# Kernel optimization log

Measured on AMD Instinct MI355X. Metric: run time of the kernel, lower is better.

Reference implementation:

```python
import jax, jax.numpy as jnp
import numpy as np

B, N, DIM, H, DH = 8, 1024, 1024, 16, 64
INNER = H * DH
GRID = 32  # 32x32 patch grid -> N=1024
EPS_LN = 1e-5
EPS_NORM = 1e-12


def _rotate_half(x):
    x1, x2 = jnp.split(x, 2, axis=-1)
    return jnp.concatenate([-x2, x1], axis=-1)


def _rope_sincos(idx, dim_quarter):
    # idx: [B, N] float -> sin/cos [B, 1, N, dim_half]
    inv_freq = 1.0 / (10000.0 ** (jnp.arange(dim_quarter, dtype=jnp.float32) / dim_quarter))
    theta = idx[..., None] * inv_freq  # [B, N, dq]
    sin = jnp.concatenate([jnp.sin(theta), jnp.sin(theta)], axis=-1)[:, None]
    cos = jnp.concatenate([jnp.cos(theta), jnp.cos(theta)], axis=-1)[:, None]
    return sin, cos


def _apply_2d_rope(q, k, h_idx, w_idx):
    D = q.shape[-1]
    dh, dq = D // 2, D // 4
    sin_h, cos_h = _rope_sincos(h_idx, dq)
    sin_w, cos_w = _rope_sincos(w_idx, dq)
    rope = lambda x, s, c: x * c + _rotate_half(x) * s
    q = jnp.concatenate([rope(q[..., :dh], sin_h, cos_h), rope(q[..., dh:], sin_w, cos_w)], axis=-1)
    k = jnp.concatenate([rope(k[..., :dh], sin_h, cos_h), rope(k[..., dh:], sin_w, cos_w)], axis=-1)
    return q, k


def setup_inputs() -> dict:
    key = jax.random.key(0)
    ks = jax.random.split(key, 8)
    x = jax.random.normal(ks[0], (B, N, DIM), dtype=jnp.float32)
    mask = jnp.ones((B, N), dtype=bool)
    ii = jnp.arange(N, dtype=jnp.float32)
    h_idx = jnp.broadcast_to(jnp.floor(ii / GRID), (B, N))
    w_idx = jnp.broadcast_to(jnp.mod(ii, GRID), (B, N))
    s = 1.0 / np.sqrt(DIM)
    return {
        "x": x,
        "mask": mask,
        "h_idx": h_idx,
        "w_idx": w_idx,
        "gamma_ln": jnp.ones((DIM,), jnp.float32),
        "beta_ln": jnp.zeros((DIM,), jnp.float32),
        "q_gamma": jnp.ones((H, 1, DH), jnp.float32),
        "k_gamma": jnp.ones((H, 1, DH), jnp.float32),
        "Wq": jax.random.normal(ks[1], (DIM, INNER), jnp.float32) * s,
        "Wkv": jax.random.normal(ks[2], (DIM, 2 * INNER), jnp.float32) * s,
        "Wo": jax.random.normal(ks[3], (INNER, DIM), jnp.float32) * s,
    }


def reference(x, mask, h_idx, w_idx, gamma_ln, beta_ln, q_gamma, k_gamma, Wq, Wkv, Wo):
    # LayerNorm (eps=1e-5, torch default)
    mu = jnp.mean(x, axis=-1, keepdims=True)
    var = jnp.var(x, axis=-1, keepdims=True)
    xn = (x - mu) * jax.lax.rsqrt(var + EPS_LN) * gamma_ln + beta_ln

    q = xn @ Wq                          # [B, N, inner]
    kv = xn @ Wkv
    k, v = jnp.split(kv, 2, axis=-1)
    split_heads = lambda t: t.reshape(B, N, H, DH).transpose(0, 2, 1, 3)  # [B,H,N,D]
    q, k, v = split_heads(q), split_heads(k), split_heads(v)

    # QK RMSNorm: F.normalize(x, dim=-1) * sqrt(D) * gamma
    scale = jnp.sqrt(jnp.float32(DH))
    l2 = lambda t: t / jnp.maximum(jnp.linalg.norm(t, axis=-1, keepdims=True), EPS_NORM)
    q = l2(q) * scale * q_gamma
    k = l2(k) * scale * k_gamma

    q, k = _apply_2d_rope(q, k, h_idx, w_idx)

    dots = jnp.einsum("bhnd,bhmd->bhnm", q, k)  # note: no 1/sqrt(d) scaling, as in source
    neg = -jnp.finfo(dots.dtype).max
    dots = jnp.where(mask[:, None, None, :], dots, neg)
    attn = jax.nn.softmax(dots, axis=-1)
    out = jnp.einsum("bhnm,bhmd->bhnd", attn, v)
    out = out.transpose(0, 2, 1, 3).reshape(B, N, INNER)
    return out @ Wo
```

## Files before the change

### kernel.cpp

```cpp
#include <hip/hip_runtime.h>
#include <math.h>


typedef float f32x4 __attribute__((ext_vector_type(4)));
typedef _Float16 f16x8 __attribute__((ext_vector_type(8)));
typedef _Float16 f16x4 __attribute__((ext_vector_type(4)));

#define MFMA16(a, b, c) __builtin_amdgcn_mfma_f32_16x16x32_f16(a, b, c, 0, 0, 0)

__device__ __forceinline__ void gl_lds16(const void* g, void* l) {
  __builtin_amdgcn_global_load_lds(
      (const __attribute__((address_space(1))) unsigned int*)g,
      (__attribute__((address_space(3))) unsigned int*)l, 16, 0, 0);
}

__global__ __launch_bounds__(256) void ln_kernel(
    const float* __restrict__ x, const float* __restrict__ gamma,
    const float* __restrict__ beta, _Float16* __restrict__ xn) {
  int row = blockIdx.x;
  const float* xr = x + (size_t)row * 1024;
  int t = threadIdx.x;
  f32x4 v = *(const f32x4*)(xr + t * 4);
  float s = v.x + v.y + v.z + v.w;
  float s2 = v.x * v.x + v.y * v.y + v.z * v.z + v.w * v.w;
#pragma unroll
  for (int off = 1; off < 64; off <<= 1) {
    s += __shfl_xor(s, off);
    s2 += __shfl_xor(s2, off);
  }
  __shared__ float red[8];
  int w = t >> 6;
  if ((t & 63) == 0) { red[w] = s; red[4 + w] = s2; }
  __syncthreads();
  s = red[0] + red[1] + red[2] + red[3];
  s2 = red[4] + red[5] + red[6] + red[7];
  float mu = s * (1.0f / 1024.0f);
  float var = s2 * (1.0f / 1024.0f) - mu * mu;
  float rs = rsqrtf(var + 1e-5f);
  f32x4 g = *(const f32x4*)(gamma + t * 4);
  f32x4 bt = *(const f32x4*)(beta + t * 4);
  f16x4 o;
  o[0] = (_Float16)((v.x - mu) * rs * g.x + bt.x);
  o[1] = (_Float16)((v.y - mu) * rs * g.y + bt.y);
  o[2] = (_Float16)((v.z - mu) * rs * g.z + bt.z);
  o[3] = (_Float16)((v.w - mu) * rs * g.w + bt.w);
  *(f16x4*)(xn + (size_t)row * 1024 + t * 4) = o;
}

__global__ __launch_bounds__(256) void transpose_f16(
    const float* __restrict__ W, _Float16* __restrict__ BT, int K, int N) {
  __shared__ _Float16 t[64][65];
  int n0 = blockIdx.x * 64, k0 = blockIdx.y * 64;
  for (int i = threadIdx.x; i < 4096; i += 256) {
    int r = i >> 6, c = i & 63;
    t[c][r] = (_Float16)W[(size_t)(k0 + r) * N + n0 + c];
  }
  __syncthreads();
  for (int i = threadIdx.x; i < 4096; i += 256) {
    int r = i >> 6, c = i & 63;
    BT[(size_t)(n0 + r) * K + k0 + c] = t[r][c];
  }
}

template <int MODE>
__global__ __launch_bounds__(256, 4) void gemm128(
    const _Float16* __restrict__ A, const _Float16* __restrict__ BT,
    float* __restrict__ Cout,
    const float* __restrict__ q_gamma, const float* __restrict__ k_gamma,
    const float* __restrict__ h_idx, const float* __restrict__ w_idx,
    _Float16* __restrict__ Qh, _Float16* __restrict__ Kh,
    _Float16* __restrict__ VT) {
  __shared__ char smem[32768];
  int tid = threadIdx.x;
  int w = tid >> 6, l = tid & 63, hi = l >> 4, lo = l & 15;
  int wm = w >> 1, wn = w & 1;
  int bcol = blockIdx.x * 128, brow = blockIdx.y * 128;
  const char* Ab = (const char*)A + (size_t)brow * 2048;
  const char* Bb = (const char*)BT + (size_t)bcol * 2048;

  auto STAGE = [&](int buf, int kt) {
    char* Ad = smem + buf * 8192;
    char* Bd = smem + 16384 + buf * 8192;
#pragma unroll
    for (int i = 0; i < 2; ++i) {
      int o = i * 4096 + w * 1024 + l * 16;
      int r = o >> 6, cb = o & 63;
      int cs = cb ^ (((r >> 1) & 3) << 4);
      gl_lds16(Ab + (size_t)r * 2048 + kt * 64 + cs, Ad + i * 4096 + w * 1024);
      gl_lds16(Bb + (size_t)r * 2048 + kt * 64 + cs, Bd + i * 4096 + w * 1024);
    }
  };

  f32x4 acc[4][4] = {};
  STAGE(0, 0);
  __syncthreads();
  for (int t = 0; t < 32; ++t) {
    int buf = t & 1;
    if (t < 31) STAGE(buf ^ 1, t + 1);
    const char* Ac = smem + buf * 8192;
    const char* Bc = smem + 16384 + buf * 8192;
    f16x8 af[4], bf[4];
#pragma unroll
    for (int m = 0; m < 4; ++m) {
      int ro = wm * 64 + m * 16 + lo;
      af[m] = *(const f16x8*)(Ac + ro * 64 + ((hi ^ ((ro >> 1) & 3)) << 4));
    }
#pragma unroll
    for (int n = 0; n < 4; ++n) {
      int ro = wn * 64 + n * 16 + lo;
      bf[n] = *(const f16x8*)(Bc + ro * 64 + ((hi ^ ((ro >> 1) & 3)) << 4));
    }
    __builtin_amdgcn_s_setprio(1);
#pragma unroll
    for (int m = 0; m < 4; ++m)
#pragma unroll
      for (int n = 0; n < 4; ++n)
        acc[m][n] = MFMA16(af[m], bf[n], acc[m][n]);
    __builtin_amdgcn_s_setprio(0);
    __syncthreads();
  }

  if constexpr (MODE == 0) {
#pragma unroll
    for (int m = 0; m < 4; ++m) {
      int r0 = brow + wm * 64 + m * 16 + hi * 4;
#pragma unroll
      for (int n = 0; n < 4; ++n) {
        int cc = bcol + wn * 64 + n * 16 + lo;
#pragma unroll
        for (int r = 0; r < 4; ++r)
          Cout[(size_t)(r0 + r) * 1024 + cc] = acc[m][n][r];
      }
    }
  } else {
    int gcol0 = bcol + wn * 64;
    if (gcol0 < 2048) {
      int head = (gcol0 & 1023) >> 6;
      const float* gm = (gcol0 < 1024 ? q_gamma : k_gamma) + head * 64;
      _Float16* dst = (gcol0 < 1024) ? Qh : Kh;
      float g0 = gm[lo], g1 = gm[16 + lo], g2 = gm[32 + lo], g3 = gm[48 + lo];
      float invf = exp2f(-13.2877123795f * (float)lo * (1.0f / 16.0f));
#pragma unroll
      for (int mf = 0; mf < 4; ++mf) {
#pragma unroll
        for (int r = 0; r < 4; ++r) {
          float v0 = acc[mf][0][r], v1 = acc[mf][1][r];
          float v2 = acc[mf][2][r], v3 = acc[mf][3][r];
          float ss = v0 * v0 + v1 * v1 + v2 * v2 + v3 * v3;
          ss += __shfl_xor(ss, 1);
          ss += __shfl_xor(ss, 2);
          ss += __shfl_xor(ss, 4);
          ss += __shfl_xor(ss, 8);
          float sc = 8.0f / fmaxf(sqrtf(ss), 1e-12f);
          float y0 = v0 * sc * g0, y1 = v1 * sc * g1;
          float y2 = v2 * sc * g2, y3 = v3 * sc * g3;
          int rr = brow + wm * 64 + mf * 16 + hi * 4 + r;
          int b = rr >> 10, tok = rr & 1023;
          float hv = h_idx[(b << 10) + tok], wv = w_idx[(b << 10) + tok];
          float sh, ch, sw2, cw;
          __sincosf(hv * invf, &sh, &ch);
          __sincosf(wv * invf, &sw2, &cw);
          _Float16* outp = dst + ((size_t)((b * 16 + head) * 1024 + tok)) * 64;
          outp[lo]      = (_Float16)(y0 * ch - y1 * sh);
          outp[16 + lo] = (_Float16)(y1 * ch + y0 * sh);
          outp[32 + lo] = (_Float16)(y2 * cw - y3 * sw2);
          outp[48 + lo] = (_Float16)(y3 * cw + y2 * sw2);
        }
      }
    } else {
      int head = (gcol0 - 2048) >> 6;
#pragma unroll
      for (int mf = 0; mf < 4; ++mf) {
        int rr0 = brow + wm * 64 + mf * 16 + hi * 4;
        int b = rr0 >> 10, tok0 = rr0 & 1023;
#pragma unroll
        for (int nf = 0; nf < 4; ++nf) {
          int d = nf * 16 + lo;
          f16x4 pk;
          pk[0] = (_Float16)acc[mf][nf][0];
          pk[1] = (_Float16)acc[mf][nf][1];
          pk[2] = (_Float16)acc[mf][nf][2];
          pk[3] = (_Float16)acc[mf][nf][3];
          *(f16x4*)(VT + ((size_t)((b * 16 + head) * 64 + d)) * 1024 + tok0) = pk;
        }
      }
    }
  }
}

__global__ __launch_bounds__(256) void flash_kernel(
    const _Float16* __restrict__ Q, const _Float16* __restrict__ Kb,
    const _Float16* __restrict__ VT, _Float16* __restrict__ AO) {
  __shared__ _Float16 Ks[2][64 * 64];
  __shared__ _Float16 Vs[2][64 * 64];
  __shared__ _Float16 Ps[4][16 * 64];
  int tid = threadIdx.x, w = tid >> 6, l = tid & 63, hi = l >> 4, lo = l & 15;
  int qt = blockIdx.x, h = blockIdx.y, b = blockIdx.z;
  int bh = (b << 4) + h;
  const _Float16* Qb = Q + (size_t)bh * 65536;
  const char* Kg = (const char*)(Kb + (size_t)bh * 65536);
  const char* Vg = (const char*)(VT + (size_t)bh * 65536);
  int qrow = qt * 64 + w * 16 + lo;
  f16x8 qf[2];
  qf[0] = *(const f16x8*)(Qb + (size_t)qrow * 64 + hi * 8);
  qf[1] = *(const f16x8*)(Qb + (size_t)qrow * 64 + 32 + hi * 8);

  int o0 = w * 1024 + l * 16;
  auto STAGE = [&](int buf, int kt) {
#pragma unroll
    for (int c = 0; c < 2; ++c) {
      int o = o0 + c * 4096;
      int row = o >> 7, col = o & 127;
      int sw = (row & 7) << 4;
      gl_lds16(Kg + (size_t)(kt * 64 + row) * 128 + (col ^ sw),
               (char*)Ks[buf] + o);
      gl_lds16(Vg + (size_t)kt * 128 + (size_t)row * 2048 + (col ^ sw),
               (char*)Vs[buf] + o);
    }
  };

  f32x4 oacc[4] = {};
  float mrun = -1e30f, lrun = 0.f;
  char* myP = (char*)Ps[w];
  int psw = (lo & 7) << 4;

  STAGE(0, 0);
  __syncthreads();
  for (int kt = 0; kt < 16; ++kt) {
    int buf = kt & 1;
    if (kt < 15) STAGE(buf ^ 1, kt + 1);
    f32x4 sacc[4] = {};
    __builtin_amdgcn_s_setprio(1);
#pragma unroll
    for (int ks = 0; ks < 2; ++ks) {
#pragma unroll
      for (int n = 0; n < 4; ++n) {
        int row = n * 16 + lo;
        f16x8 kf = *(const f16x8*)((const char*)Ks[buf] + row * 128 +
                                   ((ks * 64 + hi * 16) ^ ((row & 7) << 4)));
        sacc[n] = MFMA16(kf, qf[ks], sacc[n]);
      }
    }
    __builtin_amdgcn_s_setprio(0);
    float pmax = sacc[0][0];
#pragma unroll
    for (int n = 0; n < 4; ++n)
#pragma unroll
      for (int r = 0; r < 4; ++r) pmax = fmaxf(pmax, sacc[n][r]);
    pmax = fmaxf(pmax, __shfl_xor(pmax, 16));
    pmax = fmaxf(pmax, __shfl_xor(pmax, 32));
    float al = 1.0f;
    if (!__all(pmax <= mrun + 8.0f)) {
      float mnew = fmaxf(mrun, pmax);
      al = __expf(mrun - mnew);
      mrun = mnew;
#pragma unroll
      for (int n = 0; n < 4; ++n)
#pragma unroll
        for (int r = 0; r < 4; ++r) oacc[n][r] *= al;
    }
    float psum = 0.f;
    float p[4][4];
#pragma unroll
    for (int n = 0; n < 4; ++n)
#pragma unroll
      for (int r = 0; r < 4; ++r) {
        p[n][r] = __expf(sacc[n][r] - mrun);
        psum += p[n][r];
      }
    psum += __shfl_xor(psum, 16);
    psum += __shfl_xor(psum, 32);
    lrun = lrun * al + psum;
#pragma unroll
    for (int n = 0; n < 4; ++n) {
      f16x4 pk;
      pk[0] = (_Float16)p[n][0];
      pk[1] = (_Float16)p[n][1];
      pk[2] = (_Float16)p[n][2];
      pk[3] = (_Float16)p[n][3];
      *(f16x4*)(myP + lo * 128 + ((n * 32 + hi * 8) ^ psw)) = pk;
    }
    __builtin_amdgcn_s_setprio(1);
#pragma unroll
    for (int m = 0; m < 2; ++m) {
      f16x8 pb = *(const f16x8*)(myP + lo * 128 + ((m * 64 + hi * 16) ^ psw));
#pragma unroll
      for (int n = 0; n < 4; ++n) {
        int row = n * 16 + lo;
        f16x8 vf = *(const f16x8*)((const char*)Vs[buf] + row * 128 +
                                   ((m * 64 + hi * 16) ^ ((row & 7) << 4)));
        oacc[n] = MFMA16(vf, pb, oacc[n]);
      }
    }
    __builtin_amdgcn_s_setprio(0);
    __syncthreads();
  }
  float inv = 1.0f / lrun;
  int tok = qt * 64 + w * 16 + lo;
#pragma unroll
  for (int n = 0; n < 4; ++n) {
    f16x4 o4;
    o4[0] = (_Float16)(oacc[n][0] * inv);
    o4[1] = (_Float16)(oacc[n][1] * inv);
    o4[2] = (_Float16)(oacc[n][2] * inv);
    o4[3] = (_Float16)(oacc[n][3] * inv);
    *(f16x4*)(AO + ((size_t)(b * 1024) + tok) * 1024 + h * 64 + n * 16 + hi * 4) = o4;
  }
}

extern "C" void kernel_launch(void* const* d_in, const int* in_sizes, int n_in,
                              void* d_out, int out_size, void* d_ws, size_t ws_size,
                              hipStream_t stream) {
  const float* x        = (const float*)d_in[0];
  const float* h_idx    = (const float*)d_in[2];
  const float* w_idx    = (const float*)d_in[3];
  const float* gamma_ln = (const float*)d_in[4];
  const float* beta_ln  = (const float*)d_in[5];
  const float* q_gamma  = (const float*)d_in[6];
  const float* k_gamma  = (const float*)d_in[7];
  const float* Wq       = (const float*)d_in[8];
  const float* Wkv      = (const float*)d_in[9];
  const float* Wo       = (const float*)d_in[10];
  float* out = (float*)d_out;

  char* ws = (char*)d_ws;
  _Float16* xn     = (_Float16*)(ws);
  _Float16* BT_all = (_Float16*)(ws + 16777216);
  _Float16* Wo_bt  = (_Float16*)(ws + 23068672);
  _Float16* Qh     = (_Float16*)(ws + 25165824);
  _Float16* Kh     = (_Float16*)(ws + 41943040);
  _Float16* VTh    = (_Float16*)(ws + 58720256);
  _Float16* AO     = xn;

  ln_kernel<<<dim3(8192), dim3(256), 0, stream>>>(x, gamma_ln, beta_ln, xn);
  transpose_f16<<<dim3(16, 16), dim3(256), 0, stream>>>(Wq, BT_all, 1024, 1024);
  transpose_f16<<<dim3(32, 16), dim3(256), 0, stream>>>(
      Wkv, BT_all + 1024 * 1024, 1024, 2048);
  transpose_f16<<<dim3(16, 16), dim3(256), 0, stream>>>(Wo, Wo_bt, 1024, 1024);
  gemm128<1><<<dim3(24, 64), dim3(256), 0, stream>>>(
      xn, BT_all, nullptr, q_gamma, k_gamma, h_idx, w_idx, Qh, Kh, VTh);
  flash_kernel<<<dim3(16, 16, 8), dim3(256), 0, stream>>>(Qh, Kh, VTh, AO);
  gemm128<0><<<dim3(8, 64), dim3(256), 0, stream>>>(
      AO, Wo_bt, out, nullptr, nullptr, nullptr, nullptr, nullptr, nullptr, nullptr);
}
```

Baseline: 199.4 us.

## Merge LayerNorm and weight transposes into one launch; remap workgroups for XCD locality

Folds the LayerNorm kernel and the three weight transpose/convert kernels into a single prep kernel, so four launches become one. It also remaps 1D workgroup IDs in both GEMMs and the flash kernel so that workgroups scheduled on the same XCD (round-robin by ID mod 8) handle contiguous tiles or heads. The aim is to cut launch overhead and improve L2 reuse of shared A/B tiles and K/V per head. Mixing LN and transpose blocks in one grid can unbalance the work, and the remap assumes 8 XCDs with round-robin dispatch.

Result: faster. 188.8 us (-5.3%).

```diff
diff --git a/kernel.cpp b/kernel.cpp
--- a/kernel.cpp
+++ b/kernel.cpp
@@ -14,51 +14,64 @@
       (__attribute__((address_space(3))) unsigned int*)l, 16, 0, 0);
 }
 
-__global__ __launch_bounds__(256) void ln_kernel(
-    const float* __restrict__ x, const float* __restrict__ gamma,
-    const float* __restrict__ beta, _Float16* __restrict__ xn) {
-  int row = blockIdx.x;
-  const float* xr = x + (size_t)row * 1024;
-  int t = threadIdx.x;
-  f32x4 v = *(const f32x4*)(xr + t * 4);
-  float s = v.x + v.y + v.z + v.w;
-  float s2 = v.x * v.x + v.y * v.y + v.z * v.z + v.w * v.w;
-#pragma unroll
-  for (int off = 1; off < 64; off <<= 1) {
-    s += __shfl_xor(s, off);
-    s2 += __shfl_xor(s2, off);
-  }
+__global__ __launch_bounds__(256) void prep_kernel(
+    const float* __restrict__ x, const float* __restrict__ gamma_ln,
+    const float* __restrict__ beta_ln, _Float16* __restrict__ xn,
+    const float* __restrict__ Wq, const float* __restrict__ Wkv,
+    const float* __restrict__ Wo, _Float16* __restrict__ BT_all,
+    _Float16* __restrict__ Wo_bt) {
   __shared__ float red[8];
-  int w = t >> 6;
-  if ((t & 63) == 0) { red[w] = s; red[4 + w] = s2; }
-  __syncthreads();
-  s = red[0] + red[1] + red[2] + red[3];
-  s2 = red[4] + red[5] + red[6] + red[7];
-  float mu = s * (1.0f / 1024.0f);
-  float var = s2 * (1.0f / 1024.0f) - mu * mu;
-  float rs = rsqrtf(var + 1e-5f);
-  f32x4 g = *(const f32x4*)(gamma + t * 4);
-  f32x4 bt = *(const f32x4*)(beta + t * 4);
-  f16x4 o;
-  o[0] = (_Float16)((v.x - mu) * rs * g.x + bt.x);
-  o[1] = (_Float16)((v.y - mu) * rs * g.y + bt.y);
-  o[2] = (_Float16)((v.z - mu) * rs * g.z + bt.z);
-  o[3] = (_Float16)((v.w - mu) * rs * g.w + bt.w);
-  *(f16x4*)(xn + (size_t)row * 1024 + t * 4) = o;
-}
-
-__global__ __launch_bounds__(256) void transpose_f16(
-    const float* __restrict__ W, _Float16* __restrict__ BT, int K, int N) {
-  __shared__ _Float16 t[64][65];
-  int n0 = blockIdx.x * 64, k0 = blockIdx.y * 64;
-  for (int i = threadIdx.x; i < 4096; i += 256) {
-    int r = i >> 6, c = i & 63;
-    t[c][r] = (_Float16)W[(size_t)(k0 + r) * N + n0 + c];
-  }
-  __syncthreads();
-  for (int i = threadIdx.x; i < 4096; i += 256) {
-    int r = i >> 6, c = i & 63;
-    BT[(size_t)(n0 + r) * K + k0 + c] = t[r][c];
+  __shared__ _Float16 tb[64][65];
+  int bid = blockIdx.x, t = threadIdx.x;
+  if (bid < 8192) {
+    const float* xr = x + (size_t)bid * 1024;
+    f32x4 v = *(const f32x4*)(xr + t * 4);
+    float s = v.x + v.y + v.z + v.w;
+    float s2 = v.x * v.x + v.y * v.y + v.z * v.z + v.w * v.w;
+#pragma unroll
+    for (int off = 1; off < 64; off <<= 1) {
+      s += __shfl_xor(s, off);
+      s2 += __shfl_xor(s2, off);
+    }
+    int w = t >> 6;
+    if ((t & 63) == 0) { red[w] = s; red[4 + w] = s2; }
+    __syncthreads();
+    s = red[0] + red[1] + red[2] + red[3];
+    s2 = red[4] + red[5] + red[6] + red[7];
+    float mu = s * (1.0f / 1024.0f);
+    float var = s2 * (1.0f / 1024.0f) - mu * mu;
+    float rs = rsqrtf(var + 1e-5f);
+    f32x4 g = *(const f32x4*)(gamma_ln + t * 4);
+    f32x4 bt = *(const f32x4*)(beta_ln + t * 4);
+    f16x4 o;
+    o[0] = (_Float16)((v.x - mu) * rs * g.x + bt.x);
+    o[1] = (_Float16)((v.y - mu) * rs * g.y + bt.y);
+    o[2] = (_Float16)((v.z - mu) * rs * g.z + bt.z);
+    o[3] = (_Float16)((v.w - mu) * rs * g.w + bt.w);
+    *(f16x4*)(xn + (size_t)bid * 1024 + t * 4) = o;
+  } else {
+    int u = bid - 8192;
+    const float* W;
+    _Float16* BT;
+    int N, n0, k0;
+    if (u < 256) {
+      W = Wq; BT = BT_all; N = 1024; n0 = (u & 15) << 6; k0 = (u >> 4) << 6;
+    } else if (u < 768) {
+      int v2 = u - 256;
+      W = Wkv; BT = BT_all + 1048576; N = 2048; n0 = (v2 & 31) << 6; k0 = (v2 >> 5) << 6;
+    } else {
+      int v2 = u - 768;
+      W = Wo; BT = Wo_bt; N = 1024; n0 = (v2 & 15) << 6; k0 = (v2 >> 4) << 6;
+    }
+    for (int i = t; i < 4096; i += 256) {
+      int r = i >> 6, c = i & 63;
+      tb[c][r] = (_Float16)W[(size_t)(k0 + r) * N + n0 + c];
+    }
+    __syncthreads();
+    for (int i = t; i < 4096; i += 256) {
+      int r = i >> 6, c = i & 63;
+      BT[(size_t)(n0 + r) * 1024 + k0 + c] = tb[r][c];
+    }
   }
 }
 
@@ -71,10 +84,15 @@
     _Float16* __restrict__ Qh, _Float16* __restrict__ Kh,
     _Float16* __restrict__ VT) {
   __shared__ char smem[32768];
+  constexpr int CPX = (MODE == 1) ? 192 : 64;
+  constexpr int TX = (MODE == 1) ? 24 : 8;
+  int wg = blockIdx.x;
+  int tile = (wg & 7) * CPX + (wg >> 3);
+  int bx = tile % TX, by = tile / TX;
   int tid = threadIdx.x;
   int w = tid >> 6, l = tid & 63, hi = l >> 4, lo = l & 15;
   int wm = w >> 1, wn = w & 1;
-  int bcol = blockIdx.x * 128, brow = blockIdx.y * 128;
+  int bcol = bx * 128, brow = by * 128;
   const char* Ab = (const char*)A + (size_t)brow * 2048;
   const char* Bb = (const char*)BT + (size_t)bcol * 2048;
 
@@ -194,9 +212,11 @@
   __shared__ _Float16 Ks[2][64 * 64];
   __shared__ _Float16 Vs[2][64 * 64];
   __shared__ _Float16 Ps[4][16 * 64];
+  int wg = blockIdx.x;
+  int lin = (wg & 7) * 256 + (wg >> 3);
+  int qt = lin & 15, bh = lin >> 4;
+  int h = bh & 15, b = bh >> 4;
   int tid = threadIdx.x, w = tid >> 6, l = tid & 63, hi = l >> 4, lo = l & 15;
-  int qt = blockIdx.x, h = blockIdx.y, b = blockIdx.z;
-  int bh = (b << 4) + h;
   const _Float16* Qb = Q + (size_t)bh * 65536;
   const char* Kg = (const char*)(Kb + (size_t)bh * 65536);
   const char* Vg = (const char*)(VT + (size_t)bh * 65536);
@@ -332,14 +352,11 @@
   _Float16* VTh    = (_Float16*)(ws + 58720256);
   _Float16* AO     = xn;
 
-  ln_kernel<<<dim3(8192), dim3(256), 0, stream>>>(x, gamma_ln, beta_ln, xn);
-  transpose_f16<<<dim3(16, 16), dim3(256), 0, stream>>>(Wq, BT_all, 1024, 1024);
-  transpose_f16<<<dim3(32, 16), dim3(256), 0, stream>>>(
-      Wkv, BT_all + 1024 * 1024, 1024, 2048);
-  transpose_f16<<<dim3(16, 16), dim3(256), 0, stream>>>(Wo, Wo_bt, 1024, 1024);
-  gemm128<1><<<dim3(24, 64), dim3(256), 0, stream>>>(
+  prep_kernel<<<dim3(9216), dim3(256), 0, stream>>>(
+      x, gamma_ln, beta_ln, xn, Wq, Wkv, Wo, BT_all, Wo_bt);
+  gemm128<1><<<dim3(1536), dim3(256), 0, stream>>>(
       xn, BT_all, nullptr, q_gamma, k_gamma, h_idx, w_idx, Qh, Kh, VTh);
-  flash_kernel<<<dim3(16, 16, 8), dim3(256), 0, stream>>>(Qh, Kh, VTh, AO);
-  gemm128<0><<<dim3(8, 64), dim3(256), 0, stream>>>(
+  flash_kernel<<<dim3(2048), dim3(256), 0, stream>>>(Qh, Kh, VTh, AO);
+  gemm128<0><<<dim3(512), dim3(256), 0, stream>>>(
       AO, Wo_bt, out, nullptr, nullptr, nullptr, nullptr, nullptr, nullptr, nullptr);
 }
```
